# Performance work log

Hardware: AMD Instinct MI355X
Metric: run time of the kernel (lower is better)

The kernel has to match this reference:

```python
import jax, jax.numpy as jnp
import numpy as np

B, L, D = 2, 2048, 2048
N, K, H = 16, 8, 128
EPS = 1e-6
ROPE_THETA = 1000000
K_MASK = -2.3819763e+38


def rms_norm(x, w, eps=EPS):
    dtype = x.dtype
    rms = jnp.sqrt(jnp.mean(x.astype(jnp.float32) ** 2, axis=-1, keepdims=True) + eps)
    return (w * x / rms).astype(dtype)


def apply_rope(inputs, positions, head_dim, rope_theta=ROPE_THETA):
    # inputs: [B, L, n, H], positions: [B, L]
    fraction = 2 * jnp.arange(0, head_dim // 2, dtype=jnp.float32) / head_dim
    timescale = rope_theta ** fraction  # [H/2]
    sinusoid = positions[..., jnp.newaxis] / timescale[jnp.newaxis, jnp.newaxis, :]  # [B,L,H/2]
    sinusoid = sinusoid[..., jnp.newaxis, :]  # [B,L,1,H/2]
    sin, cos = jnp.sin(sinusoid), jnp.cos(sinusoid)
    first, second = jnp.split(inputs, 2, axis=-1)
    out = jnp.concatenate([first * cos - second * sin, second * cos + first * sin], axis=-1)
    return out.astype(inputs.dtype)


def setup_inputs() -> dict:
    key = jax.random.key(0)
    ks = jax.random.split(key, 6)
    x = jax.random.normal(ks[0], (B, L, D), dtype=jnp.float32)
    position_ids = jnp.broadcast_to(jnp.arange(L, dtype=jnp.int32)[None, :], (B, L))
    # causal mask [B, L, S]
    attn_mask = jnp.broadcast_to(jnp.tril(jnp.ones((L, L), dtype=bool))[None], (B, L, L))
    wq = jax.random.normal(ks[1], (D, N, H), dtype=jnp.float32) * 0.02
    wk = jax.random.normal(ks[2], (D, K, H), dtype=jnp.float32) * 0.02
    wv = jax.random.normal(ks[3], (D, K, H), dtype=jnp.float32) * 0.02
    wo = jax.random.normal(ks[4], (N, H, D), dtype=jnp.float32) * 0.02
    q_norm_w = jnp.ones((H,), dtype=jnp.float32)
    k_norm_w = jnp.ones((H,), dtype=jnp.float32)
    return {"x": x, "position_ids": position_ids, "attn_mask": attn_mask,
            "wq": wq, "wk": wk, "wv": wv, "wo": wo,
            "q_norm_w": q_norm_w, "k_norm_w": k_norm_w}


def reference(x, position_ids, attn_mask, wq, wk, wv, wo, q_norm_w, k_norm_w):
    scale = H ** (-0.5)
    q = jnp.einsum('BLD,DNH->BLNH', x, wq)  # [B,L,N,H]
    k = jnp.einsum('BSD,DKH->BSKH', x, wk)  # [B,S,K,H]
    v = jnp.einsum('BSD,DKH->BSKH', x, wv)
    q = rms_norm(q, q_norm_w)
    k = rms_norm(k, k_norm_w)
    q = apply_rope(q, position_ids, H)
    k = apply_rope(k, position_ids, H)
    b, l, n, h = q.shape
    s = k.shape[1]
    kk = k.shape[2]
    q = q.reshape((b, l, kk, n // kk, h))
    attn = jnp.einsum('BLKGH,BSKH->BKGLS', q, k) * scale
    attn = attn.reshape((b, n, l, s))
    attn = jnp.where(jnp.expand_dims(attn_mask, -3), attn, K_MASK)
    attn = jax.nn.softmax(attn.astype(jnp.float32), axis=-1).astype(k.dtype)
    attn = attn.reshape((b, kk, n // kk, l, s))
    qkv = jnp.einsum('BKGLS,BSKH->BLKGH', attn, v).reshape((b, l, n, h))
    out = jnp.einsum('BLNH,NHD->BLD', qkv, wo)
    return out
```

## Files before the change

kernel.cpp:

```cpp
#include <hip/hip_runtime.h>

#define B_ 2
#define L_ 2048
#define D_ 2048
#define NH_ 16
#define KH_ 8
#define HD_ 128

typedef __attribute__((ext_vector_type(8))) short short8;
typedef __attribute__((ext_vector_type(4))) short short4v;
typedef __attribute__((ext_vector_type(4))) float floatx4;

__device__ __forceinline__ unsigned short f2bf(float f) {
  unsigned u = __float_as_uint(f);
  unsigned r = (u + 0x7fffu + ((u >> 16) & 1u)) >> 16;
  return (unsigned short)r;
}
__device__ __forceinline__ float bf2f(unsigned short h) {
  return __uint_as_float(((unsigned)h) << 16);
}
__device__ __forceinline__ void gl_lds16(const void* g, void* l) {
  __builtin_amdgcn_global_load_lds(
      (const __attribute__((address_space(1))) unsigned int*)g,
      (__attribute__((address_space(3))) unsigned int*)l, 16, 0, 0);
}
__device__ __forceinline__ void barrier_lds_only() {
  asm volatile("s_waitcnt lgkmcnt(0)" ::: "memory");
  __builtin_amdgcn_s_barrier();
}

__global__ __launch_bounds__(256) void prep1(const float* __restrict__ x,
                                             const float* __restrict__ wq,
                                             const float* __restrict__ wk,
                                             const float* __restrict__ wv,
                                             const float* __restrict__ wo,
                                             unsigned short* __restrict__ xb,
                                             unsigned short* __restrict__ wqkv_t,
                                             unsigned short* __restrict__ wo_t) {
  int id = blockIdx.x;
  int t = threadIdx.x;
  if (id < 8192) {
    long i = ((long)id * 256 + t) * 4;
    float4 v = *(const float4*)(x + i);
    ushort4 o;
    o.x = f2bf(v.x); o.y = f2bf(v.y); o.z = f2bf(v.z); o.w = f2bf(v.w);
    *(ushort4*)(xb + i) = o;
    return;
  }
  id -= 8192;
  __shared__ float tile[32][33];
  const float* in;
  unsigned short* out;
  int C, sh;
  if (id < 4096) {
    in = wq; out = wqkv_t; C = 2048; sh = 6;
  } else if (id < 6144) {
    in = wk; out = wqkv_t + 2048L * 2048; C = 1024; sh = 5; id -= 4096;
  } else if (id < 8192) {
    in = wv; out = wqkv_t + 3072L * 2048; C = 1024; sh = 5; id -= 6144;
  } else {
    in = wo; out = wo_t; C = 2048; sh = 6; id -= 8192;
  }
  int c0 = (id & ((1 << sh) - 1)) * 32, r0 = (id >> sh) * 32;
  int tx = t & 31, ty = t >> 5;
#pragma unroll
  for (int i = 0; i < 4; i++)
    tile[ty + i * 8][tx] = in[(long)(r0 + ty + i * 8) * C + c0 + tx];
  __syncthreads();
#pragma unroll
  for (int i = 0; i < 4; i++) {
    int oc = ty + i * 8;
    out[(long)(c0 + oc) * 2048 + r0 + tx] = f2bf(tile[tx][oc]);
  }
}

__global__ __launch_bounds__(256) void prep2(const unsigned short* __restrict__ qkv,
                                             const int* __restrict__ pos,
                                             const float* __restrict__ qw,
                                             const float* __restrict__ kw,
                                             unsigned short* __restrict__ qo,
                                             unsigned short* __restrict__ ko,
                                             unsigned short* __restrict__ vT) {
  int id = blockIdx.x;
  int t = threadIdx.x;
  if (id < 24576) {
    const int lane = t & 63, w = t >> 6;
    const int gid = id * 4 + w;
    const int row = gid / 24;
    const int hd = gid - row * 24;
    const int b = row >> 11, l = row & 2047;
    const unsigned short* src = qkv + (long)row * 4096 + hd * 128;
    float x0 = bf2f(src[lane]);
    float x1 = bf2f(src[lane + 64]);
    float ss = x0 * x0 + x1 * x1;
#pragma unroll
    for (int off = 32; off; off >>= 1) ss += __shfl_xor(ss, off);
    float inv = 1.0f / sqrtf(ss * (1.0f / 128.0f) + 1e-6f);
    const float* nw = (hd < 16) ? qw : kw;
    x0 = nw[lane] * x0 * inv;
    x1 = nw[lane + 64] * x1 * inv;
    float p = (float)pos[row];
    float ang = p * exp2f((float)lane * -0.31143075889f);
    float s, c;
    sincosf(ang, &s, &c);
    float o0 = x0 * c - x1 * s;
    float o1 = x1 * c + x0 * s;
    unsigned short* dst;
    if (hd < 16) {
      const float QSC = 0.08838834764831845f * 1.4426950408889634f;
      o0 *= QSC;
      o1 *= QSC;
      dst = qo + (((long)b * NH_ + hd) * L_ + l) * HD_;
    } else {
      dst = ko + (((long)b * KH_ + (hd - 16)) * L_ + l) * HD_;
    }
    dst[lane] = f2bf(o0);
    dst[lane + 64] = f2bf(o1);
    return;
  }
  id -= 24576;
  __shared__ unsigned short tile[32][33];
  int l0 = (id & 63) * 32, h0 = ((id >> 6) & 3) * 32;
  int bk = id >> 8;
  int b = bk >> 3, kh = bk & 7;
  int tx = t & 31, ty = t >> 5;
  const unsigned short* src = qkv + (long)b * L_ * 4096 + 3072 + kh * 128;
#pragma unroll
  for (int i = 0; i < 4; i++)
    tile[ty + i * 8][tx] = src[(long)(l0 + ty + i * 8) * 4096 + h0 + tx];
  __syncthreads();
  unsigned short* dst = vT + (long)bk * HD_ * L_;
#pragma unroll
  for (int i = 0; i < 4; i++)
    dst[(long)(h0 + ty + i * 8) * L_ + l0 + tx] = tile[tx][ty + i * 8];
}

template <int MODE>
__global__ __launch_bounds__(256, 3) void gemm128(const unsigned short* __restrict__ A,
                                                  const unsigned short* __restrict__ Bt,
                                                  void* __restrict__ C,
                                                  int M, int N, int K) {
  __shared__ unsigned short As[128 * 64];
  __shared__ unsigned short Bs[128 * 64];
  const int t = threadIdx.x;
  const int lane = t & 63, w = t >> 6;
  const int wy = w >> 1, wx = w & 1;
  const int col = lane & 15, quad = lane >> 4;
  const long m0 = (long)blockIdx.y * 128, n0 = (long)blockIdx.x * 128;
  floatx4 acc[4][4];
#pragma unroll
  for (int i = 0; i < 4; i++)
#pragma unroll
    for (int j = 0; j < 4; j++) acc[i][j] = (floatx4)0.0f;
  const int rs = t >> 3, bs = t & 7;
  for (int kt = 0; kt < K; kt += 64) {
#pragma unroll
    for (int i = 0; i < 4; i++) {
      int r = i * 32 + rs;
      gl_lds16(A + (m0 + r) * (long)K + kt + ((bs ^ (r & 7)) << 3),
               &As[(i * 32 + w * 8) * 64]);
      gl_lds16(Bt + (n0 + r) * (long)K + kt + ((bs ^ (r & 7)) << 3),
               &Bs[(i * 32 + w * 8) * 64]);
    }
    __syncthreads();
#pragma unroll
    for (int ks = 0; ks < 2; ks++) {
      short8 af[4], bf[4];
#pragma unroll
      for (int mi = 0; mi < 4; mi++) {
        int row = wy * 64 + mi * 16 + col;
        int blk = ks * 4 + quad;
        af[mi] = *(const short8*)&As[row * 64 + ((blk ^ (row & 7)) << 3)];
      }
#pragma unroll
      for (int ni = 0; ni < 4; ni++) {
        int row = wx * 64 + ni * 16 + col;
        int blk = ks * 4 + quad;
        bf[ni] = *(const short8*)&Bs[row * 64 + ((blk ^ (row & 7)) << 3)];
      }
#pragma unroll
      for (int mi = 0; mi < 4; mi++)
#pragma unroll
        for (int ni = 0; ni < 4; ni++)
          acc[mi][ni] = __builtin_amdgcn_mfma_f32_16x16x32_bf16(af[mi], bf[ni],
                                                                acc[mi][ni], 0, 0, 0);
    }
    __syncthreads();
  }
#pragma unroll
  for (int mi = 0; mi < 4; mi++)
#pragma unroll
    for (int r = 0; r < 4; r++) {
      long row = m0 + wy * 64 + mi * 16 + quad * 4 + r;
#pragma unroll
      for (int ni = 0; ni < 4; ni++) {
        long cg = n0 + wx * 64 + ni * 16 + col;
        float val = acc[mi][ni][r];
        if (MODE == 1)
          ((unsigned short*)C)[row * N + cg] = f2bf(val);
        else
          ((float*)C)[row * N + cg] = val;
      }
    }
}

template <int MODE>
__global__ __launch_bounds__(512, 2) void gemm256(const unsigned short* __restrict__ A,
                                                  const unsigned short* __restrict__ Bt,
                                                  void* __restrict__ C,
                                                  int M, int N, int K) {
  __shared__ unsigned short As[2][256 * 64];
  __shared__ unsigned short Bs[2][256 * 64];
  const int t = threadIdx.x;
  const int lane = t & 63, w = t >> 6;
  const int wy = w >> 2, wx = w & 3;
  const int col = lane & 15, quad = lane >> 4;
  const long m0 = (long)blockIdx.y * 256, n0 = (long)blockIdx.x * 256;
  const int rs = t >> 3, bs = t & 7;
  const int nt = K >> 6;

#define SA256(bufi, Tt, h)                                                      \
  gl_lds16(A + (m0 + (h) * 64 + rs) * (long)K + (long)(Tt) * 64 +               \
               ((bs ^ (rs & 7)) << 3),                                          \
           &As[bufi][((h) * 64 + w * 8) * 64])
#define SB256(bufi, Tt, h)                                                      \
  gl_lds16(Bt + (n0 + (h) * 64 + rs) * (long)K + (long)(Tt) * 64 +              \
                ((bs ^ (rs & 7)) << 3),                                         \
           &Bs[bufi][((h) * 64 + w * 8) * 64])

  floatx4 acc[8][4];
#pragma unroll
  for (int i = 0; i < 8; i++)
#pragma unroll
    for (int j = 0; j < 4; j++) acc[i][j] = (floatx4)0.0f;

  SA256(0, 0, 0); SA256(0, 0, 1); SA256(0, 0, 2); SA256(0, 0, 3);
  SB256(0, 0, 0); SB256(0, 0, 1); SB256(0, 0, 2); SB256(0, 0, 3);
  SB256(1, 1, 0); SB256(1, 1, 1); SB256(1, 1, 2); SB256(1, 1, 3);
  asm volatile("s_waitcnt vmcnt(4)" ::: "memory");
  __builtin_amdgcn_s_barrier();

  for (int T = 0; T < nt; ++T) {
    const int c = T & 1;
    const unsigned short* Ac = As[c];
    const unsigned short* Bc = Bs[c];
    short8 a[4][2], b[4][2];

#pragma unroll
    for (int mi = 0; mi < 4; mi++)
#pragma unroll
      for (int ks = 0; ks < 2; ks++) {
        int row = wy * 128 + mi * 16 + col;
        a[mi][ks] = *(const short8*)&Ac[row * 64 + (((ks * 4 + quad) ^ (row & 7)) << 3)];
      }
#pragma unroll
    for (int ni = 0; ni < 2; ni++)
#pragma unroll
      for (int ks = 0; ks < 2; ks++) {
        int row = wx * 64 + ni * 16 + col;
        b[ni][ks] = *(const short8*)&Bc[row * 64 + (((ks * 4 + quad) ^ (row & 7)) << 3)];
      }
    if (T + 1 < nt) { SA256(c ^ 1, T + 1, 0); SA256(c ^ 1, T + 1, 2); }
    __builtin_amdgcn_s_barrier();
    asm volatile("s_waitcnt lgkmcnt(0)" ::: "memory");
    __builtin_amdgcn_s_setprio(1);
#pragma unroll
    for (int mi = 0; mi < 4; mi++)
#pragma unroll
      for (int ni = 0; ni < 2; ni++)
#pragma unroll
        for (int ks = 0; ks < 2; ks++)
          acc[mi][ni] = __builtin_amdgcn_mfma_f32_16x16x32_bf16(a[mi][ks], b[ni][ks],
                                                                acc[mi][ni], 0, 0, 0);
    __builtin_amdgcn_s_setprio(0);
    __builtin_amdgcn_s_barrier();

#pragma unroll
    for (int ni = 2; ni < 4; ni++)
#pragma unroll
      for (int ks = 0; ks < 2; ks++) {
        int row = wx * 64 + ni * 16 + col;
        b[ni][ks] = *(const short8*)&Bc[row * 64 + (((ks * 4 + quad) ^ (row & 7)) << 3)];
      }
    if (T + 1 < nt) { SA256(c ^ 1, T + 1, 1); SA256(c ^ 1, T + 1, 3); }
    __builtin_amdgcn_s_barrier();
    asm volatile("s_waitcnt lgkmcnt(0)" ::: "memory");
    __builtin_amdgcn_s_setprio(1);
#pragma unroll
    for (int mi = 0; mi < 4; mi++)
#pragma unroll
      for (int ni = 2; ni < 4; ni++)
#pragma unroll
        for (int ks = 0; ks < 2; ks++)
          acc[mi][ni] = __builtin_amdgcn_mfma_f32_16x16x32_bf16(a[mi][ks], b[ni][ks],
                                                                acc[mi][ni], 0, 0, 0);
    __builtin_amdgcn_s_setprio(0);
    __builtin_amdgcn_s_barrier();

#pragma unroll
    for (int mi = 0; mi < 4; mi++)
#pragma unroll
      for (int ks = 0; ks < 2; ks++) {
        int row = wy * 128 + (mi + 4) * 16 + col;
        a[mi][ks] = *(const short8*)&Ac[row * 64 + (((ks * 4 + quad) ^ (row & 7)) << 3)];
      }
    if (T + 2 < nt) { SB256(c, T + 2, 0); SB256(c, T + 2, 1); }
    __builtin_amdgcn_s_barrier();
    asm volatile("s_waitcnt lgkmcnt(0)" ::: "memory");
    __builtin_amdgcn_s_setprio(1);
#pragma unroll
    for (int mi = 0; mi < 4; mi++)
#pragma unroll
      for (int ni = 0; ni < 2; ni++)
#pragma unroll
        for (int ks = 0; ks < 2; ks++)
          acc[mi + 4][ni] = __builtin_amdgcn_mfma_f32_16x16x32_bf16(a[mi][ks], b[ni][ks],
                                                                    acc[mi + 4][ni], 0, 0, 0);
    __builtin_amdgcn_s_setprio(0);
    __builtin_amdgcn_s_barrier();

    if (T + 2 < nt) { SB256(c, T + 2, 2); SB256(c, T + 2, 3); }
    __builtin_amdgcn_s_setprio(1);
#pragma unroll
    for (int mi = 0; mi < 4; mi++)
#pragma unroll
      for (int ni = 2; ni < 4; ni++)
#pragma unroll
        for (int ks = 0; ks < 2; ks++)
          acc[mi + 4][ni] = __builtin_amdgcn_mfma_f32_16x16x32_bf16(a[mi][ks], b[ni][ks],
                                                                    acc[mi + 4][ni], 0, 0, 0);
    __builtin_amdgcn_s_setprio(0);
    if (T + 1 < nt) {
      if (T >= nt - 2)
        asm volatile("s_waitcnt vmcnt(0)" ::: "memory");
      else
        asm volatile("s_waitcnt vmcnt(4)" ::: "memory");
      __builtin_amdgcn_s_barrier();
    }
  }
#undef SA256
#undef SB256

#pragma unroll
  for (int mi = 0; mi < 8; mi++)
#pragma unroll
    for (int r = 0; r < 4; r++) {
      long row = m0 + wy * 128 + mi * 16 + quad * 4 + r;
#pragma unroll
      for (int ni = 0; ni < 4; ni++) {
        long cg = n0 + wx * 64 + ni * 16 + col;
        float val = acc[mi][ni][r];
        if (MODE == 1)
          ((unsigned short*)C)[row * N + cg] = f2bf(val);
        else
          ((float*)C)[row * N + cg] = val;
      }
    }
}

__global__ __launch_bounds__(256, 2) void flash(const unsigned short* __restrict__ Q,
                                                const unsigned short* __restrict__ Kg,
                                                const unsigned short* __restrict__ VT,
                                                unsigned short* __restrict__ Og) {
  __shared__ unsigned short Ks[64 * 128];
  __shared__ unsigned short Vs[128 * 64];
  __shared__ unsigned short Ps[128 * 72];
  const int n = blockIdx.y, b = blockIdx.z;
  const int qt = b ? (15 - blockIdx.x) : blockIdx.x;
  const int t = threadIdx.x, lane = t & 63, w = t >> 6;
  const int col = lane & 15, quad = lane >> 4;
  const int kvh = n >> 1;
  const unsigned short* kb = Kg + ((long)b * KH_ + kvh) * L_ * HD_;
  const unsigned short* vtb = VT + ((long)b * KH_ + kvh) * HD_ * L_;
  const int l0 = qt * 128;
  const int steps = 2 * qt + 2;
  const unsigned short* qb = Q + (((long)b * NH_ + n) * L_ + l0) * HD_;

  const int rK = t >> 4, blkK = t & 15;
  const int rV = t >> 3, blkV = t & 7;

  short8 qf[2][4];
#pragma unroll
  for (int mi = 0; mi < 2; mi++)
#pragma unroll
    for (int ks = 0; ks < 4; ks++)
      qf[mi][ks] = *(const short8*)(qb + (w * 32 + mi * 16 + col) * 128 + ks * 32 + quad * 8);

  floatx4 o[2][8];
#pragma unroll
  for (int mi = 0; mi < 2; mi++)
#pragma unroll
    for (int nf = 0; nf < 8; nf++) o[mi][nf] = (floatx4)0.0f;
  float lrow[2] = {0.0f, 0.0f};

  {
#pragma unroll
    for (int i = 0; i < 4; i++) {
      int r = i * 16 + rK;
      int gblk = (blkK & 8) | ((blkK ^ r) & 7);
      gl_lds16(kb + (long)r * 128 + gblk * 8, &Ks[(i * 16 + w * 4) * 128]);
    }
#pragma unroll
    for (int j = 0; j < 4; j++) {
      int r = j * 32 + rV;
      int gblk = (blkV ^ r) & 7;
      gl_lds16(vtb + (long)r * L_ + gblk * 8, &Vs[(j * 32 + w * 8) * 64]);
    }
  }
  __syncthreads();

  short8 kpre[4], vpre[4];
  if (steps > 1) {
    const int s0n = 64;
#pragma unroll
    for (int i = 0; i < 4; i++) {
      int r = i * 16 + rK;
      int gblk = (blkK & 8) | ((blkK ^ r) & 7);
      kpre[i] = *(const short8*)(kb + (long)(s0n + r) * 128 + gblk * 8);
    }
#pragma unroll
    for (int j = 0; j < 4; j++) {
      int r = j * 32 + rV;
      int gblk = (blkV ^ r) & 7;
      vpre[j] = *(const short8*)(vtb + (long)r * L_ + s0n + gblk * 8);
    }
  }

  for (int st = 0; st < steps; st++) {
    const int s0 = st * 64;

    floatx4 sa[2][4];
#pragma unroll
    for (int mi = 0; mi < 2; mi++)
#pragma unroll
      for (int sf = 0; sf < 4; sf++) sa[mi][sf] = (floatx4)0.0f;
#pragma unroll
    for (int ks = 0; ks < 4; ks++) {
      short8 bf[4];
#pragma unroll
      for (int sf = 0; sf < 4; sf++) {
        int srow = sf * 16 + col;
        int blk = ks * 4 + quad;
        bf[sf] = *(const short8*)&Ks[srow * 128 + (((blk & 8) | ((blk ^ srow) & 7)) << 3)];
      }
#pragma unroll
      for (int mi = 0; mi < 2; mi++)
#pragma unroll
        for (int sf = 0; sf < 4; sf++)
          sa[mi][sf] = __builtin_amdgcn_mfma_f32_16x16x32_bf16(bf[sf], qf[mi][ks],
                                                               sa[mi][sf], 0, 0, 0);
    }

    if (st >= steps - 2) {
#pragma unroll
      for (int mi = 0; mi < 2; mi++) {
        int lg = l0 + w * 32 + mi * 16 + col;
#pragma unroll
        for (int sf = 0; sf < 4; sf++)
#pragma unroll
          for (int r = 0; r < 4; r++) {
            int sg = s0 + sf * 16 + quad * 4 + r;
            if (sg > lg) sa[mi][sf][r] = -3.0e38f;
          }
      }
    }

#pragma unroll
    for (int mi = 0; mi < 2; mi++)
#pragma unroll
      for (int sf = 0; sf < 4; sf++) {
        short4v pk;
#pragma unroll
        for (int r = 0; r < 4; r++) {
          float pv = exp2f(sa[mi][sf][r] - 17.0f);
          lrow[mi] += pv;
          pk[r] = (short)f2bf(pv);
        }
        *(short4v*)&Ps[(w * 32 + mi * 16 + col) * 72 + sf * 16 + quad * 4] = pk;
      }

#pragma unroll
    for (int ks = 0; ks < 2; ks++) {
      short8 pf[2];
#pragma unroll
      for (int mi = 0; mi < 2; mi++)
        pf[mi] = *(const short8*)&Ps[(w * 32 + mi * 16 + col) * 72 + ks * 32 + quad * 8];
      short8 vf[8];
#pragma unroll
      for (int nf = 0; nf < 8; nf++) {
        int h = nf * 16 + col;
        int blk = ks * 4 + quad;
        vf[nf] = *(const short8*)&Vs[h * 64 + ((blk ^ (h & 7)) << 3)];
      }
#pragma unroll
      for (int mi = 0; mi < 2; mi++)
#pragma unroll
        for (int nf = 0; nf < 8; nf++)
          o[mi][nf] = __builtin_amdgcn_mfma_f32_16x16x32_bf16(pf[mi], vf[nf],
                                                              o[mi][nf], 0, 0, 0);
    }

    barrier_lds_only();
    if (st + 1 < steps) {
#pragma unroll
      for (int i = 0; i < 4; i++) {
        int r = i * 16 + rK;
        *(short8*)&Ks[r * 128 + blkK * 8] = kpre[i];
      }
#pragma unroll
      for (int j = 0; j < 4; j++) {
        int r = j * 32 + rV;
        *(short8*)&Vs[r * 64 + blkV * 8] = vpre[j];
      }
      barrier_lds_only();
      if (st + 2 < steps) {
        const int s0n = (st + 2) * 64;
#pragma unroll
        for (int i = 0; i < 4; i++) {
          int r = i * 16 + rK;
          int gblk = (blkK & 8) | ((blkK ^ r) & 7);
          kpre[i] = *(const short8*)(kb + (long)(s0n + r) * 128 + gblk * 8);
        }
#pragma unroll
        for (int j = 0; j < 4; j++) {
          int r = j * 32 + rV;
          int gblk = (blkV ^ r) & 7;
          vpre[j] = *(const short8*)(vtb + (long)r * L_ + s0n + gblk * 8);
        }
      }
    }
  }

#pragma unroll
  for (int mi = 0; mi < 2; mi++) {
    float s = lrow[mi];
    s += __shfl_xor(s, 16);
    s += __shfl_xor(s, 32);
#pragma unroll
    for (int r = 0; r < 4; r++) {
      float inv = 1.0f / __shfl(s, quad * 4 + r);
      int lg = l0 + w * 32 + mi * 16 + quad * 4 + r;
      unsigned short* dst = Og + (((long)b * L_ + lg) * NH_ + n) * HD_;
#pragma unroll
      for (int nf = 0; nf < 8; nf++)
        dst[nf * 16 + col] = f2bf(o[mi][nf][r] * inv);
    }
  }
}

extern "C" void kernel_launch(void* const* d_in, const int* in_sizes, int n_in,
                              void* d_out, int out_size, void* d_ws, size_t ws_size,
                              hipStream_t stream) {
  const float* x = (const float*)d_in[0];
  const int* pos = (const int*)d_in[1];
  const float* wq = (const float*)d_in[3];
  const float* wk = (const float*)d_in[4];
  const float* wv = (const float*)d_in[5];
  const float* wo = (const float*)d_in[6];
  const float* qnw = (const float*)d_in[7];
  const float* knw = (const float*)d_in[8];
  float* out = (float*)d_out;

  char* ws = (char*)d_ws;
  unsigned short* xb     = (unsigned short*)(ws + 0);
  unsigned short* wqkv_t = (unsigned short*)(ws + 16777216);
  unsigned short* wo_t   = (unsigned short*)(ws + 33554432);
  unsigned short* qkv    = (unsigned short*)(ws + 41943040);
  unsigned short* q      = (unsigned short*)(ws + 75497472);
  unsigned short* k      = (unsigned short*)(ws + 92274688);
  unsigned short* vT     = (unsigned short*)(ws + 100663296);
  unsigned short* ao     = (unsigned short*)(ws + 109051904);
  if (ws_size < 125829120) return;

  prep1<<<20480, 256, 0, stream>>>(x, wq, wk, wv, wo, xb, wqkv_t, wo_t);
  gemm256<1><<<dim3(16, 16), 512, 0, stream>>>(xb, wqkv_t, qkv, 4096, 4096, 2048);
  prep2<<<28672, 256, 0, stream>>>(qkv, pos, qnw, knw, q, k, vT);
  flash<<<dim3(16, NH_, B_), 256, 0, stream>>>(q, k, vT, ao);
  gemm128<0><<<dim3(16, 32), 256, 0, stream>>>(ao, wo_t, out, 4096, 2048, 2048);
}
```

Baseline: 347.3 us.

## Split long causal query tiles across two KV chunks with a combine pass

Query tiles 8-15 are now each split into two blocks that process halves of the KV range, raising the flash grid from 16 to 24 blocks per head. The split blocks write unnormalized fp32 partial outputs and row sums into reused workspace, and a new combine kernel sums and normalizes them into bf16. The aim is better load balance and more parallelism for the long causal tiles. The cost is an extra kernel launch and fp32 partial traffic. The removed batch-dependent tile reversal also changes block scheduling order.

```diff
diff --git a/kernel.cpp b/kernel.cpp
--- a/kernel.cpp
+++ b/kernel.cpp
@@ -361,19 +361,31 @@
 __global__ __launch_bounds__(256, 2) void flash(const unsigned short* __restrict__ Q,
                                                 const unsigned short* __restrict__ Kg,
                                                 const unsigned short* __restrict__ VT,
-                                                unsigned short* __restrict__ Og) {
+                                                unsigned short* __restrict__ Og,
+                                                float* __restrict__ Opart,
+                                                float* __restrict__ lpart) {
   __shared__ unsigned short Ks[64 * 128];
   __shared__ unsigned short Vs[128 * 64];
   __shared__ unsigned short Ps[128 * 72];
   const int n = blockIdx.y, b = blockIdx.z;
-  const int qt = b ? (15 - blockIdx.x) : blockIdx.x;
+  const int slot = blockIdx.x;
+  int qt, st0, st1, chunk;
+  if (slot < 8) {
+    qt = slot; chunk = -1; st0 = 0; st1 = 2 * qt + 2;
+  } else {
+    qt = 8 + ((slot - 8) >> 1);
+    chunk = (slot - 8) & 1;
+    const int half = qt + 1;
+    st0 = chunk ? half : 0;
+    st1 = chunk ? 2 * half : half;
+  }
+  const int steps_full = 2 * qt + 2;
   const int t = threadIdx.x, lane = t & 63, w = t >> 6;
   const int col = lane & 15, quad = lane >> 4;
   const int kvh = n >> 1;
   const unsigned short* kb = Kg + ((long)b * KH_ + kvh) * L_ * HD_;
   const unsigned short* vtb = VT + ((long)b * KH_ + kvh) * HD_ * L_;
   const int l0 = qt * 128;
-  const int steps = 2 * qt + 2;
   const unsigned short* qb = Q + (((long)b * NH_ + n) * L_ + l0) * HD_;
 
   const int rK = t >> 4, blkK = t & 15;
@@ -394,29 +406,30 @@
   float lrow[2] = {0.0f, 0.0f};
 
   {
+    const long sb = (long)st0 * 64;
 #pragma unroll
     for (int i = 0; i < 4; i++) {
       int r = i * 16 + rK;
       int gblk = (blkK & 8) | ((blkK ^ r) & 7);
-      gl_lds16(kb + (long)r * 128 + gblk * 8, &Ks[(i * 16 + w * 4) * 128]);
+      gl_lds16(kb + (sb + r) * 128 + gblk * 8, &Ks[(i * 16 + w * 4) * 128]);
     }
 #pragma unroll
     for (int j = 0; j < 4; j++) {
       int r = j * 32 + rV;
       int gblk = (blkV ^ r) & 7;
-      gl_lds16(vtb + (long)r * L_ + gblk * 8, &Vs[(j * 32 + w * 8) * 64]);
+      gl_lds16(vtb + (long)r * L_ + sb + gblk * 8, &Vs[(j * 32 + w * 8) * 64]);
     }
   }
   __syncthreads();
 
   short8 kpre[4], vpre[4];
-  if (steps > 1) {
-    const int s0n = 64;
+  if (st0 + 1 < st1) {
+    const long s0n = (long)(st0 + 1) * 64;
 #pragma unroll
     for (int i = 0; i < 4; i++) {
       int r = i * 16 + rK;
       int gblk = (blkK & 8) | ((blkK ^ r) & 7);
-      kpre[i] = *(const short8*)(kb + (long)(s0n + r) * 128 + gblk * 8);
+      kpre[i] = *(const short8*)(kb + (s0n + r) * 128 + gblk * 8);
     }
 #pragma unroll
     for (int j = 0; j < 4; j++) {
@@ -426,7 +439,7 @@
     }
   }
 
-  for (int st = 0; st < steps; st++) {
+  for (int st = st0; st < st1; st++) {
     const int s0 = st * 64;
 
     floatx4 sa[2][4];
@@ -451,7 +464,7 @@
                                                                sa[mi][sf], 0, 0, 0);
     }
 
-    if (st >= steps - 2) {
+    if (st >= steps_full - 2) {
 #pragma unroll
       for (int mi = 0; mi < 2; mi++) {
         int lg = l0 + w * 32 + mi * 16 + col;
@@ -501,7 +514,7 @@
     }
 
     barrier_lds_only();
-    if (st + 1 < steps) {
+    if (st + 1 < st1) {
 #pragma unroll
       for (int i = 0; i < 4; i++) {
         int r = i * 16 + rK;
@@ -513,13 +526,13 @@
         *(short8*)&Vs[r * 64 + blkV * 8] = vpre[j];
       }
       barrier_lds_only();
-      if (st + 2 < steps) {
-        const int s0n = (st + 2) * 64;
+      if (st + 2 < st1) {
+        const long s0n = (long)(st + 2) * 64;
 #pragma unroll
         for (int i = 0; i < 4; i++) {
           int r = i * 16 + rK;
           int gblk = (blkK & 8) | ((blkK ^ r) & 7);
-          kpre[i] = *(const short8*)(kb + (long)(s0n + r) * 128 + gblk * 8);
+          kpre[i] = *(const short8*)(kb + (s0n + r) * 128 + gblk * 8);
         }
 #pragma unroll
         for (int j = 0; j < 4; j++) {
@@ -531,20 +544,65 @@
     }
   }
 
-#pragma unroll
-  for (int mi = 0; mi < 2; mi++) {
-    float s = lrow[mi];
-    s += __shfl_xor(s, 16);
-    s += __shfl_xor(s, 32);
-#pragma unroll
-    for (int r = 0; r < 4; r++) {
-      float inv = 1.0f / __shfl(s, quad * 4 + r);
-      int lg = l0 + w * 32 + mi * 16 + quad * 4 + r;
-      unsigned short* dst = Og + (((long)b * L_ + lg) * NH_ + n) * HD_;
-#pragma unroll
-      for (int nf = 0; nf < 8; nf++)
-        dst[nf * 16 + col] = f2bf(o[mi][nf][r] * inv);
-    }
+  if (chunk < 0) {
+#pragma unroll
+    for (int mi = 0; mi < 2; mi++) {
+      float s = lrow[mi];
+      s += __shfl_xor(s, 16);
+      s += __shfl_xor(s, 32);
+#pragma unroll
+      for (int r = 0; r < 4; r++) {
+        float inv = 1.0f / __shfl(s, quad * 4 + r);
+        int lg = l0 + w * 32 + mi * 16 + quad * 4 + r;
+        unsigned short* dst = Og + (((long)b * L_ + lg) * NH_ + n) * HD_;
+#pragma unroll
+        for (int nf = 0; nf < 8; nf++)
+          dst[nf * 16 + col] = f2bf(o[mi][nf][r] * inv);
+      }
+    }
+  } else {
+    const int pidx = (((b * NH_ + n) * 8) + (qt - 8)) * 2 + chunk;
+    float* Od = Opart + (long)pidx * 16384;
+#pragma unroll
+    for (int mi = 0; mi < 2; mi++) {
+      float s = lrow[mi];
+      s += __shfl_xor(s, 16);
+      s += __shfl_xor(s, 32);
+      if (lane < 16) lpart[pidx * 128 + w * 32 + mi * 16 + lane] = s;
+#pragma unroll
+      for (int r = 0; r < 4; r++) {
+        int rl = w * 32 + mi * 16 + quad * 4 + r;
+#pragma unroll
+        for (int nf = 0; nf < 8; nf++)
+          Od[rl * 128 + nf * 16 + col] = o[mi][nf][r];
+      }
+    }
+  }
+}
+
+__global__ __launch_bounds__(256) void combine(const float* __restrict__ Opart,
+                                               const float* __restrict__ lpart,
+                                               unsigned short* __restrict__ Og) {
+  const int id = blockIdx.x;
+  const int q8 = id & 7, n = (id >> 3) & 15, b = id >> 7;
+  const int pidx = (((b * NH_ + n) * 8) + q8) * 2;
+  const float* OA = Opart + (long)pidx * 16384;
+  const float* OB = OA + 16384;
+  const int t = threadIdx.x;
+  const int r = t >> 1, c0 = (t & 1) * 64;
+  const float inv = 1.0f / (lpart[pidx * 128 + r] + lpart[(pidx + 1) * 128 + r]);
+  const int lg = (8 + q8) * 128 + r;
+  unsigned short* dst = Og + (((long)b * L_ + lg) * NH_ + n) * HD_ + c0;
+#pragma unroll
+  for (int c = 0; c < 64; c += 4) {
+    float4 a = *(const float4*)(OA + r * 128 + c0 + c);
+    float4 bb = *(const float4*)(OB + r * 128 + c0 + c);
+    ushort4 ov;
+    ov.x = f2bf((a.x + bb.x) * inv);
+    ov.y = f2bf((a.y + bb.y) * inv);
+    ov.z = f2bf((a.z + bb.z) * inv);
+    ov.w = f2bf((a.w + bb.w) * inv);
+    *(ushort4*)(dst + c) = ov;
   }
 }
 
@@ -572,9 +630,13 @@
   unsigned short* ao     = (unsigned short*)(ws + 109051904);
   if (ws_size < 125829120) return;
 
+  float* Opart = (float*)qkv;
+  float* lpart = (float*)xb;
+
   prep1<<<20480, 256, 0, stream>>>(x, wq, wk, wv, wo, xb, wqkv_t, wo_t);
   gemm256<1><<<dim3(16, 16), 512, 0, stream>>>(xb, wqkv_t, qkv, 4096, 4096, 2048);
   prep2<<<28672, 256, 0, stream>>>(qkv, pos, qnw, knw, q, k, vT);
-  flash<<<dim3(16, NH_, B_), 256, 0, stream>>>(q, k, vT, ao);
+  flash<<<dim3(24, NH_, B_), 256, 0, stream>>>(q, k, vT, ao, Opart, lpart);
+  combine<<<256, 256, 0, stream>>>(Opart, lpart, ao);
   gemm128<0><<<dim3(16, 32), 256, 0, stream>>>(ao, wo_t, out, 4096, 2048, 2048);
 }
```

After: 370.6 us. 1.07x slower.
